# Kernel optimization log

Measured on AMD Instinct MI355X. Metric: run time of the kernel, lower is better.

## Reference

```python
import jax, jax.numpy as jnp
import numpy as np

B, S, D, H, MLP = 8, 1024, 768, 12, 3072
HD = D // H
EPS = 1e-5


def setup_inputs() -> dict:
    key = jax.random.key(0)
    ks = jax.random.split(key, 5)
    sd = lambda fan_in: 1.0 / np.sqrt(fan_in)
    return {
        "x": jax.random.normal(ks[0], (B, S, D), jnp.float32),
        "w_qkv": jax.random.normal(ks[1], (D, 3 * D), jnp.float32) * sd(D),
        "w_out": jax.random.normal(ks[2], (D, D), jnp.float32) * sd(D),
        "b_out": jnp.zeros((D,), jnp.float32),
        "w1": jax.random.normal(ks[3], (D, MLP), jnp.float32) * sd(D),
        "b1": jnp.zeros((MLP,), jnp.float32),
        "w2": jax.random.normal(ks[4], (MLP, D), jnp.float32) * sd(MLP),
        "b2": jnp.zeros((D,), jnp.float32),
    }


def _instance_norm(x):
    # torch InstanceNorm2d on a 3D [B,S,D] tensor treats it as unbatched (C,H,W):
    # normalize over (S, D) per batch element, biased var, eps=1e-5, no affine.
    mu = jnp.mean(x, axis=(1, 2), keepdims=True)
    var = jnp.mean(jnp.square(x - mu), axis=(1, 2), keepdims=True)
    return (x - mu) * jax.lax.rsqrt(var + EPS)


def reference(x, w_qkv, w_out, b_out, w1, b1, w2, b2):
    scale = HD ** -0.5
    # --- self-attention branch ---
    h = _instance_norm(x)
    qkv = (h @ w_qkv).reshape(B, S, 3, H, HD)          # (qkv, heads, head_dim) split
    qkv = qkv.transpose(2, 0, 3, 1, 4)                  # [3, B, H, S, HD]
    q, k, v = qkv[0], qkv[1], qkv[2]
    att = jax.nn.softmax(jnp.einsum('bhxd,bhyd->bhxy', q, k) * scale, axis=-1)
    o = jnp.einsum('bhxy,bhyd->bhxd', att, v)           # [B, H, S, HD]
    o = o.transpose(0, 2, 1, 3).reshape(B, S, D)        # b h l d -> b l (h d)
    x = x + (o @ w_out + b_out)
    # --- MLP branch (exact erf GELU, as nn.GELU default) ---
    h2 = _instance_norm(x)
    m = jax.nn.gelu(h2 @ w1 + b1, approximate=False) @ w2 + b2
    return x + m
```

## Files before the change

kernel.cpp:

```cpp
#include <hip/hip_runtime.h>
#include <hip/hip_bf16.h>

typedef __hip_bfloat16 bf16;
typedef __attribute__((ext_vector_type(8))) short short8;
typedef __attribute__((ext_vector_type(4))) float f32x4;

#define B_   8
#define S_   1024
#define D_   768
#define H_   12
#define HD_  64
#define MLP_ 3072
#define SD_  (S_ * D_)

#define QSCALE 0.18033688011112042f

__device__ __forceinline__ float b2f(short h) {
  union { unsigned u; float f; } w;
  w.u = ((unsigned)(unsigned short)h) << 16;
  return w.f;
}

__device__ __forceinline__ void gl2lds16(const bf16* g, bf16* l) {
  __builtin_amdgcn_global_load_lds(
      (const __attribute__((address_space(1))) unsigned*)(const void*)g,
      (__attribute__((address_space(3))) unsigned*)(void*)l, 16, 0, 0);
}

__global__ __launch_bounds__(256) void transpose_all(
    const float* __restrict__ w_qkv, const float* __restrict__ w_out,
    const float* __restrict__ w1, const float* __restrict__ w2,
    bf16* __restrict__ t_qkv, bf16* __restrict__ t_out,
    bf16* __restrict__ t1, bf16* __restrict__ t2) {
  const int t = blockIdx.x;
  const float* in; bf16* out; int R, C, idx;
  if (t < 1728)      { in = w_qkv; out = t_qkv; R = 768;  C = 2304; idx = t; }
  else if (t < 2304) { in = w_out; out = t_out; R = 768;  C = 768;  idx = t - 1728; }
  else if (t < 4608) { in = w1;    out = t1;    R = 768;  C = 3072; idx = t - 2304; }
  else               { in = w2;    out = t2;    R = 3072; C = 768;  idx = t - 4608; }
  const int nbx = C >> 5;
  const int bx = (idx % nbx) * 32, by = (idx / nbx) * 32;
  __shared__ float tt[32][33];
  const int tx = threadIdx.x & 31, ty = threadIdx.x >> 5;
#pragma unroll
  for (int rr = 0; rr < 32; rr += 8)
    tt[ty + rr][tx] = in[(long)(by + ty + rr) * C + bx + tx];
  __syncthreads();
#pragma unroll
  for (int rr = 0; rr < 32; rr += 8)
    out[(long)(bx + ty + rr) * R + by + tx] = __float2bfloat16(tt[tx][ty + rr]);
}

__global__ __launch_bounds__(256) void stats_partial(const float* __restrict__ x,
                                                     float* __restrict__ redp,
                                                     const bf16* __restrict__ wt1,
                                                     const bf16* __restrict__ wt_qkv,
                                                     float* __restrict__ cs1,
                                                     float* __restrict__ csq,
                                                     bf16* __restrict__ xb) {
  if (blockIdx.x >= 768) {
    const bf16* wsrc; float* cdst; int bi;
    if (blockIdx.x < 816) { wsrc = wt1;    cdst = cs1; bi = blockIdx.x - 768; }
    else                  { wsrc = wt_qkv; cdst = csq; bi = blockIdx.x - 816; }
    const int row = bi * 64 + (threadIdx.x >> 2);
    const int part = threadIdx.x & 3;
    const bf16* wr = wsrc + (long)row * 768 + part * 192;
    float s = 0.f;
#pragma unroll
    for (int u = 0; u < 24; ++u) {
      short8 v = *(const short8*)(wr + u * 8);
#pragma unroll
      for (int e = 0; e < 8; ++e) s += b2f(v[e]);
    }
    s += __shfl_xor(s, 1, 64);
    s += __shfl_xor(s, 2, 64);
    if (part == 0) cdst[row] = s;
    return;
  }
  const long off = (long)blockIdx.x * 8192;
  float s = 0.f, s2 = 0.f;
#pragma unroll
  for (int it = 0; it < 4; ++it) {
    const long i = off + ((long)threadIdx.x + it * 256) * 8;
    float4 v0 = *(const float4*)(x + i);
    float4 v1 = *(const float4*)(x + i + 4);
    s += v0.x + v0.y + v0.z + v0.w + v1.x + v1.y + v1.z + v1.w;
    s2 += v0.x * v0.x + v0.y * v0.y + v0.z * v0.z + v0.w * v0.w +
          v1.x * v1.x + v1.y * v1.y + v1.z * v1.z + v1.w * v1.w;
    __align__(16) bf16 tmp[8];
    tmp[0] = __float2bfloat16(v0.x); tmp[1] = __float2bfloat16(v0.y);
    tmp[2] = __float2bfloat16(v0.z); tmp[3] = __float2bfloat16(v0.w);
    tmp[4] = __float2bfloat16(v1.x); tmp[5] = __float2bfloat16(v1.y);
    tmp[6] = __float2bfloat16(v1.z); tmp[7] = __float2bfloat16(v1.w);
    *(short8*)(xb + i) = *(const short8*)tmp;
  }
#pragma unroll
  for (int o = 1; o < 64; o <<= 1) { s += __shfl_xor(s, o, 64); s2 += __shfl_xor(s2, o, 64); }
  __shared__ float sh[8];
  const int wave = threadIdx.x >> 6, lane = threadIdx.x & 63;
  if (lane == 0) { sh[wave * 2] = s; sh[wave * 2 + 1] = s2; }
  __syncthreads();
  if (threadIdx.x == 0) {
    redp[blockIdx.x * 2]     = sh[0] + sh[2] + sh[4] + sh[6];
    redp[blockIdx.x * 2 + 1] = sh[1] + sh[3] + sh[5] + sh[7];
  }
}

__global__ __launch_bounds__(512) void stats_final(const float* __restrict__ redp,
                                                   float* __restrict__ red_x,
                                                   float* __restrict__ red2) {
  const int b = threadIdx.x >> 6, lane = threadIdx.x & 63;
  const int i0 = (b * 96 + lane) * 2;
  float s  = redp[i0]     + ((lane < 32) ? redp[i0 + 128]     : 0.f);
  float s2 = redp[i0 + 1] + ((lane < 32) ? redp[i0 + 128 + 1] : 0.f);
#pragma unroll
  for (int o = 1; o < 64; o <<= 1) { s += __shfl_xor(s, o, 64); s2 += __shfl_xor(s2, o, 64); }
  if (lane == 0) { red_x[b * 2] = s; red_x[b * 2 + 1] = s2; }
  if (threadIdx.x < 16) red2[threadIdx.x] = 0.f;
}

template <int EPI, bool STATS>
__global__ __launch_bounds__(256) void gemm_k(
    const bf16* __restrict__ A, const bf16* __restrict__ Bt,
    int M, int N, int K,
    const float* __restrict__ biasf, const float* __restrict__ resf,
    const float* __restrict__ cs, const float* __restrict__ stat_in,
    float* __restrict__ outf,
    bf16* __restrict__ outb0, bf16* __restrict__ outb1, bf16* __restrict__ outb2,
    float* __restrict__ statp) {
  __shared__ __align__(16) bf16 As[128 * 64];
  __shared__ __align__(16) bf16 Bs[128 * 64];
  __shared__ float sred[8];
  const int tid = threadIdx.x;
  const int bm = blockIdx.x * 128, bn = blockIdx.y * 128;
  const int wave = tid >> 6, lane = tid & 63;
  const int quad = lane >> 4, l16 = lane & 15;
  const int wm = (wave >> 1) * 64, wn = (wave & 1) * 64;
  const int swz = l16 & 7;

  f32x4 acc[4][4];
#pragma unroll
  for (int i = 0; i < 4; ++i)
#pragma unroll
    for (int j = 0; j < 4; ++j) acc[i][j] = (f32x4){0.f, 0.f, 0.f, 0.f};

  const int srow = tid >> 3;
  const int sgc = (tid & 7) ^ (srow & 7);
  const bf16* Ab = A + (long)(bm + srow) * K + sgc * 8;
  const bf16* Bb = Bt + (long)(bn + srow) * K + sgc * 8;

  auto stage = [&](int k0) {
#pragma unroll
    for (int s = 0; s < 4; ++s)
      gl2lds16(Ab + (long)(s * 32) * K + k0, &As[0] + s * 2048 + tid * 8);
#pragma unroll
    for (int s = 0; s < 4; ++s)
      gl2lds16(Bb + (long)(s * 32) * K + k0, &Bs[0] + s * 2048 + tid * 8);
  };

  stage(0);
  const int nk = K >> 6;
  for (int kt = 0; kt < nk; ++kt) {
    __syncthreads();
    short8 a[2][4], b[2][4];
#pragma unroll
    for (int kk = 0; kk < 2; ++kk) {
      const int co = ((kk * 4 + quad) ^ swz) * 8;
#pragma unroll
      for (int i = 0; i < 4; ++i)
        a[kk][i] = *(const short8*)(&As[0] + (wm + i * 16 + l16) * 64 + co);
#pragma unroll
      for (int j = 0; j < 4; ++j)
        b[kk][j] = *(const short8*)(&Bs[0] + (wn + j * 16 + l16) * 64 + co);
    }
    __syncthreads();
    if (kt + 1 < nk) stage((kt + 1) * 64);
#pragma unroll
    for (int kk = 0; kk < 2; ++kk)
#pragma unroll
      for (int i = 0; i < 4; ++i)
#pragma unroll
        for (int j = 0; j < 4; ++j)
          acc[i][j] = __builtin_amdgcn_mfma_f32_16x16x32_bf16(a[kk][i], b[kk][j], acc[i][j], 0, 0, 0);
  }

  const int m0 = bm + wm + quad * 4;
  const int n0 = bn + wn + l16;
  const int batch = bm >> 10;
  float mu = 0.f, rs = 0.f;
  if (EPI == 0 || EPI == 2) {
    const float s1 = stat_in[batch * 2], s2v = stat_in[batch * 2 + 1];
    mu = s1 * (1.0f / SD_);
    rs = rsqrtf(s2v * (1.0f / SD_) - mu * mu + 1e-5f);
  }
  float ts = 0.f, ts2 = 0.f;
#pragma unroll
  for (int i = 0; i < 4; ++i) {
#pragma unroll
    for (int j = 0; j < 4; ++j) {
      const int n = n0 + j * 16;
#pragma unroll
      for (int r = 0; r < 4; ++r) {
        const int m = m0 + i * 16 + r;
        float v = acc[i][j][r];
        if (EPI == 0) {
          v = rs * (v - mu * cs[n]);
          const int t = n / D_;
          const int rr2 = n - t * D_;
          const int hh = rr2 >> 6, dd = rr2 & 63;
          const int bb = m >> 10, ss = m & 1023;
          const long hoff = (long)(bb * H_ + hh);
          if (t == 0)      outb0[(hoff * S_ + ss) * HD_ + dd] = __float2bfloat16(v * QSCALE);
          else if (t == 1) outb1[(hoff * S_ + ss) * HD_ + dd] = __float2bfloat16(v);
          else             outb2[(hoff * HD_ + dd) * S_ + ss] = __float2bfloat16(v);
        } else if (EPI == 1) {
          v += biasf[n] + resf[(long)m * N + n];
          outf[(long)m * N + n] = v;
          outb0[(long)m * N + n] = __float2bfloat16(v);
          if (STATS) { ts += v; ts2 += v * v; }
        } else if (EPI == 2) {
          v = rs * (v - mu * cs[n]) + biasf[n];
          float u = v * v;
          float y = v * (1.0f + 0.044715f * u) * 0.7978845608028654f;
          float z = exp2f(y * -2.885390081777927f);
          v = v * __builtin_amdgcn_rcpf(1.0f + z);
          outb0[(long)m * N + n] = __float2bfloat16(v);
        } else {
          v += biasf[n] + resf[(long)m * N + n];
          outf[(long)m * N + n] = v;
        }
      }
    }
  }
  if (STATS) {
#pragma unroll
    for (int o = 1; o < 64; o <<= 1) { ts += __shfl_xor(ts, o, 64); ts2 += __shfl_xor(ts2, o, 64); }
    if (lane == 0) { sred[wave * 2] = ts; sred[wave * 2 + 1] = ts2; }
    __syncthreads();
    if (tid == 0) {
      atomicAdd(&statp[batch * 2], sred[0] + sred[2] + sred[4] + sred[6]);
      atomicAdd(&statp[batch * 2 + 1], sred[1] + sred[3] + sred[5] + sred[7]);
    }
  }
}

__global__ __launch_bounds__(512) void attn64(const bf16* __restrict__ q,
                                              const bf16* __restrict__ k,
                                              const bf16* __restrict__ vt,
                                              bf16* __restrict__ o) {
  __shared__ __align__(16) bf16 Ks[2][64 * 64];
  __shared__ __align__(16) bf16 Vs[2][64 * 64];
  __shared__ __align__(16) bf16 Ps[8 * 16 * 64];
  const int bh = blockIdx.x, qt = blockIdx.y;
  const int tid = threadIdx.x, wave = tid >> 6, lane = tid & 63;
  const int quad = lane >> 4, l16 = lane & 15;
  const int sw = (l16 & 7) ^ ((l16 >> 3) & 1);
  const long base = (long)bh * (S_ * HD_);
  const bf16* kg = k + base;
  const bf16* vg = vt + base;

  const int srow = tid >> 3;
  const int scg = (tid & 7) ^ (srow & 7) ^ ((srow >> 3) & 1);

  short8 aq[2];
#pragma unroll
  for (int kk = 0; kk < 2; ++kk)
    aq[kk] = *(const short8*)(q + base + (long)(qt * 128 + wave * 16 + l16) * HD_ +
                              kk * 32 + quad * 8);

  gl2lds16(kg + (long)srow * HD_ + scg * 8, &Ks[0][0] + tid * 8);
  gl2lds16(vg + (long)srow * S_ + scg * 8, &Vs[0][0] + tid * 8);

  const bf16* kp = kg + (long)(64 + srow) * HD_ + scg * 8;
  const bf16* vp = vg + (long)srow * S_ + 64 + scg * 8;

  f32x4 oacc[4];
#pragma unroll
  for (int j = 0; j < 4; ++j) oacc[j] = (f32x4){0.f, 0.f, 0.f, 0.f};
  float lp = 0.f;

  bf16* Pw = Ps + wave * 1024 + l16 * 64;

#define ATTN_STEP(CUR, DOPREF)                                                 \
  {                                                                            \
    __syncthreads();                                                           \
    f32x4 s[4];                                                                \
    _Pragma("unroll")                                                          \
    for (int i = 0; i < 4; ++i) s[i] = (f32x4){0.f, 0.f, 0.f, 0.f};            \
    _Pragma("unroll")                                                          \
    for (int kk = 0; kk < 2; ++kk) {                                           \
      _Pragma("unroll")                                                        \
      for (int i = 0; i < 4; ++i) {                                            \
        short8 ak = *(const short8*)(&Ks[CUR][0] + (i * 16 + l16) * 64 +       \
                                     (((kk * 4 + quad) ^ sw) * 8));            \
        s[i] = __builtin_amdgcn_mfma_f32_16x16x32_bf16(ak, aq[kk], s[i], 0, 0, 0); \
      }                                                                        \
    }                                                                          \
    if (DOPREF) {                                                              \
      gl2lds16(kp, &Ks[(CUR) ^ 1][0] + tid * 8);                               \
      gl2lds16(vp, &Vs[(CUR) ^ 1][0] + tid * 8);                               \
      kp += 64 * HD_;                                                          \
      vp += 64;                                                                \
    }                                                                          \
    _Pragma("unroll")                                                          \
    for (int i = 0; i < 4; ++i) {                                              \
      __align__(8) bf16 pk[4];                                                 \
      _Pragma("unroll")                                                        \
      for (int r = 0; r < 4; ++r) {                                            \
        float p = exp2f(s[i][r]);                                              \
        lp += p;                                                               \
        pk[r] = __float2bfloat16(p);                                           \
      }                                                                        \
      *(uint2*)(Pw + (((2 * i + (quad >> 1)) ^ sw) * 8) + (quad & 1) * 4) =    \
          *(const uint2*)pk;                                                   \
    }                                                                          \
    _Pragma("unroll")                                                          \
    for (int kk = 0; kk < 2; ++kk) {                                           \
      short8 ap = *(const short8*)(Pw + (((kk * 4 + quad) ^ sw) * 8));         \
      _Pragma("unroll")                                                        \
      for (int dj = 0; dj < 4; ++dj) {                                         \
        short8 bv = *(const short8*)(&Vs[CUR][0] + (dj * 16 + l16) * 64 +      \
                                     (((kk * 4 + quad) ^ sw) * 8));            \
        oacc[dj] = __builtin_amdgcn_mfma_f32_16x16x32_bf16(ap, bv, oacc[dj], 0, 0, 0); \
      }                                                                        \
    }                                                                          \
  }

  for (int c = 0; c < 16; c += 2) {
    ATTN_STEP(0, true)
    ATTN_STEP(1, (c < 14))
  }
#undef ATTN_STEP

  float lt = lp;
  lt += __shfl_xor(lt, 16, 64);
  lt += __shfl_xor(lt, 32, 64);

  const int b = bh / H_, hh = bh - b * H_;
#pragma unroll
  for (int r = 0; r < 4; ++r) {
    const float inv = 1.0f / __shfl(lt, quad * 4 + r, 64);
    const int sg = qt * 128 + wave * 16 + quad * 4 + r;
    const long rowoff = ((long)b * S_ + sg) * D_ + hh * HD_;
#pragma unroll
    for (int dj = 0; dj < 4; ++dj)
      o[rowoff + dj * 16 + l16] = __float2bfloat16(oacc[dj][r] * inv);
  }
}

extern "C" void kernel_launch(void* const* d_in, const int* in_sizes, int n_in,
                              void* d_out, int out_size, void* d_ws, size_t ws_size,
                              hipStream_t stream) {
  const float* x     = (const float*)d_in[0];
  const float* w_qkv = (const float*)d_in[1];
  const float* w_out = (const float*)d_in[2];
  const float* b_out = (const float*)d_in[3];
  const float* w1    = (const float*)d_in[4];
  const float* b1    = (const float*)d_in[5];
  const float* w2    = (const float*)d_in[6];
  const float* b2    = (const float*)d_in[7];
  float* out = (float*)d_out;

  bf16* wt_qkv = (bf16*)d_ws;
  bf16* wt_out = wt_qkv + 2304 * 768;
  bf16* wt1    = wt_out + 768 * 768;
  bf16* wt2    = wt1 + 3072 * 768;
  bf16* qb     = wt2 + 768 * 3072;
  bf16* kb     = qb + 6291456;
  bf16* vtb    = kb + 6291456;
  bf16* ob     = vtb + 6291456;
  float* x1f   = (float*)(ob + 6291456);
  bf16* hb     = (bf16*)(x1f + 6291456);
  float* redp  = (float*)(hb + 6291456);
  float* red_x = redp + 1536;
  float* red2  = red_x + 16;
  float* cs1   = red2 + 16;
  float* csq   = cs1 + 3072;
  bf16* gb     = qb;
  bf16* xb     = hb;
  bf16* x1b    = hb;

  transpose_all<<<6912, 256, 0, stream>>>(w_qkv, w_out, w1, w2,
                                          wt_qkv, wt_out, wt1, wt2);

  stats_partial<<<768 + 48 + 36, 256, 0, stream>>>(x, redp, wt1, wt_qkv,
                                                   cs1, csq, xb);
  stats_final<<<1, 512, 0, stream>>>(redp, red_x, red2);

  gemm_k<0, false><<<dim3(64, 18), 256, 0, stream>>>(
      xb, wt_qkv, 8192, 2304, 768, nullptr, nullptr, csq, red_x,
      nullptr, qb, kb, vtb, nullptr);
  attn64<<<dim3(B_ * H_, 8), 512, 0, stream>>>(qb, kb, vtb, ob);

  gemm_k<1, true><<<dim3(64, 6), 256, 0, stream>>>(
      ob, wt_out, 8192, 768, 768, b_out, x, nullptr, nullptr,
      x1f, x1b, nullptr, nullptr, red2);

  gemm_k<2, false><<<dim3(64, 24), 256, 0, stream>>>(
      x1b, wt1, 8192, 3072, 768, b1, nullptr, cs1, red2,
      nullptr, gb, nullptr, nullptr, nullptr);

  gemm_k<3, false><<<dim3(64, 6), 256, 0, stream>>>(
      gb, wt2, 8192, 768, 3072, b2, x1f, nullptr, nullptr,
      out, nullptr, nullptr, nullptr, nullptr);
}
```

Baseline: 333.7 us.

## Drop stats_final via atomics and keep attention P in registers

The per-batch instance-norm sums are now accumulated with atomicAdd straight from stats_partial, which removes the separate single-block stats_final launch. The zeroing of both stat buffers moves into the first transpose block. In the attention kernel, the softmax probabilities are packed directly into MFMA A-operand registers instead of round-tripping through a shared-memory P buffer. To match that register layout, V is read from LDS as two 8-byte halves. This saves LDS traffic and a small launch, at the cost of float atomics on the stats (non-deterministic summation order) and more, narrower LDS reads of V.

```diff
diff --git a/kernel.cpp b/kernel.cpp
--- a/kernel.cpp
+++ b/kernel.cpp
@@ -31,8 +31,10 @@
     const float* __restrict__ w_qkv, const float* __restrict__ w_out,
     const float* __restrict__ w1, const float* __restrict__ w2,
     bf16* __restrict__ t_qkv, bf16* __restrict__ t_out,
-    bf16* __restrict__ t1, bf16* __restrict__ t2) {
+    bf16* __restrict__ t1, bf16* __restrict__ t2,
+    float* __restrict__ zstats) {
   const int t = blockIdx.x;
+  if (t == 0 && threadIdx.x < 32) zstats[threadIdx.x] = 0.f;
   const float* in; bf16* out; int R, C, idx;
   if (t < 1728)      { in = w_qkv; out = t_qkv; R = 768;  C = 2304; idx = t; }
   else if (t < 2304) { in = w_out; out = t_out; R = 768;  C = 768;  idx = t - 1728; }
@@ -52,7 +54,7 @@
 }
 
 __global__ __launch_bounds__(256) void stats_partial(const float* __restrict__ x,
-                                                     float* __restrict__ redp,
+                                                     float* __restrict__ red_x,
                                                      const bf16* __restrict__ wt1,
                                                      const bf16* __restrict__ wt_qkv,
                                                      float* __restrict__ cs1,
@@ -101,22 +103,10 @@
   if (lane == 0) { sh[wave * 2] = s; sh[wave * 2 + 1] = s2; }
   __syncthreads();
   if (threadIdx.x == 0) {
-    redp[blockIdx.x * 2]     = sh[0] + sh[2] + sh[4] + sh[6];
-    redp[blockIdx.x * 2 + 1] = sh[1] + sh[3] + sh[5] + sh[7];
-  }
-}
-
-__global__ __launch_bounds__(512) void stats_final(const float* __restrict__ redp,
-                                                   float* __restrict__ red_x,
-                                                   float* __restrict__ red2) {
-  const int b = threadIdx.x >> 6, lane = threadIdx.x & 63;
-  const int i0 = (b * 96 + lane) * 2;
-  float s  = redp[i0]     + ((lane < 32) ? redp[i0 + 128]     : 0.f);
-  float s2 = redp[i0 + 1] + ((lane < 32) ? redp[i0 + 128 + 1] : 0.f);
-#pragma unroll
-  for (int o = 1; o < 64; o <<= 1) { s += __shfl_xor(s, o, 64); s2 += __shfl_xor(s2, o, 64); }
-  if (lane == 0) { red_x[b * 2] = s; red_x[b * 2 + 1] = s2; }
-  if (threadIdx.x < 16) red2[threadIdx.x] = 0.f;
+    const int bb = blockIdx.x / 96;
+    atomicAdd(&red_x[bb * 2],     sh[0] + sh[2] + sh[4] + sh[6]);
+    atomicAdd(&red_x[bb * 2 + 1], sh[1] + sh[3] + sh[5] + sh[7]);
+  }
 }
 
 template <int EPI, bool STATS>
@@ -250,7 +240,6 @@
                                               bf16* __restrict__ o) {
   __shared__ __align__(16) bf16 Ks[2][64 * 64];
   __shared__ __align__(16) bf16 Vs[2][64 * 64];
-  __shared__ __align__(16) bf16 Ps[8 * 16 * 64];
   const int bh = blockIdx.x, qt = blockIdx.y;
   const int tid = threadIdx.x, wave = tid >> 6, lane = tid & 63;
   const int quad = lane >> 4, l16 = lane & 15;
@@ -279,7 +268,7 @@
   for (int j = 0; j < 4; ++j) oacc[j] = (f32x4){0.f, 0.f, 0.f, 0.f};
   float lp = 0.f;
 
-  bf16* Pw = Ps + wave * 1024 + l16 * 64;
+  const int vh = (quad & 1) * 4;
 
 #define ATTN_STEP(CUR, DOPREF)                                                 \
   {                                                                            \
@@ -302,26 +291,31 @@
       kp += 64 * HD_;                                                          \
       vp += 64;                                                                \
     }                                                                          \
+    float pe[4][4];                                                            \
     _Pragma("unroll")                                                          \
     for (int i = 0; i < 4; ++i) {                                              \
-      __align__(8) bf16 pk[4];                                                 \
       _Pragma("unroll")                                                        \
-      for (int r = 0; r < 4; ++r) {                                            \
-        float p = exp2f(s[i][r]);                                              \
-        lp += p;                                                               \
-        pk[r] = __float2bfloat16(p);                                           \
-      }                                                                        \
-      *(uint2*)(Pw + (((2 * i + (quad >> 1)) ^ sw) * 8) + (quad & 1) * 4) =    \
-          *(const uint2*)pk;                                                   \
+      for (int r = 0; r < 4; ++r) { pe[i][r] = exp2f(s[i][r]); lp += pe[i][r]; } \
+    }                                                                          \
+    union { short8 v; bf16 b[8]; } af[2];                                      \
+    _Pragma("unroll")                                                          \
+    for (int r = 0; r < 4; ++r) {                                              \
+      af[0].b[r]     = __float2bfloat16(pe[0][r]);                             \
+      af[0].b[4 + r] = __float2bfloat16(pe[1][r]);                             \
+      af[1].b[r]     = __float2bfloat16(pe[2][r]);                             \
+      af[1].b[4 + r] = __float2bfloat16(pe[3][r]);                             \
     }                                                                          \
     _Pragma("unroll")                                                          \
     for (int kk = 0; kk < 2; ++kk) {                                           \
-      short8 ap = *(const short8*)(Pw + (((kk * 4 + quad) ^ sw) * 8));         \
+      const int g0 = ((4 * kk + (quad >> 1)) ^ sw) * 8 + vh;                   \
+      const int g1 = ((4 * kk + 2 + (quad >> 1)) ^ sw) * 8 + vh;               \
       _Pragma("unroll")                                                        \
       for (int dj = 0; dj < 4; ++dj) {                                         \
-        short8 bv = *(const short8*)(&Vs[CUR][0] + (dj * 16 + l16) * 64 +      \
-                                     (((kk * 4 + quad) ^ sw) * 8));            \
-        oacc[dj] = __builtin_amdgcn_mfma_f32_16x16x32_bf16(ap, bv, oacc[dj], 0, 0, 0); \
+        const bf16* vrow = &Vs[CUR][0] + (dj * 16 + l16) * 64;                 \
+        union { short8 v; uint2 u[2]; } bv;                                    \
+        bv.u[0] = *(const uint2*)(vrow + g0);                                  \
+        bv.u[1] = *(const uint2*)(vrow + g1);                                  \
+        oacc[dj] = __builtin_amdgcn_mfma_f32_16x16x32_bf16(af[kk].v, bv.v, oacc[dj], 0, 0, 0); \
       }                                                                        \
     }                                                                          \
   }
@@ -381,11 +375,10 @@
   bf16* x1b    = hb;
 
   transpose_all<<<6912, 256, 0, stream>>>(w_qkv, w_out, w1, w2,
-                                          wt_qkv, wt_out, wt1, wt2);
-
-  stats_partial<<<768 + 48 + 36, 256, 0, stream>>>(x, redp, wt1, wt_qkv,
+                                          wt_qkv, wt_out, wt1, wt2, red_x);
+
+  stats_partial<<<768 + 48 + 36, 256, 0, stream>>>(x, red_x, wt1, wt_qkv,
                                                    cs1, csq, xb);
-  stats_final<<<1, 512, 0, stream>>>(redp, red_x, red2);
 
   gemm_k<0, false><<<dim3(64, 18), 256, 0, stream>>>(
       xb, wt_qkv, 8192, 2304, 768, nullptr, nullptr, csq, red_x,
```

After: 345.5 us. +3.6%, slower.
